# Performance work log

Hardware: AMD Instinct MI355X
Metric: run time of the kernel (lower is better)

The kernel has to match this reference:

```python
import jax, jax.numpy as jnp
import numpy as np
import math

BIG, SMALL, HEADS, FF_MULT = 4096, 256, 4, 2
HEAD_DIM = SMALL // HEADS
FF = SMALL * FF_MULT
EPS = 1.1920929e-07  # torch.nn.RMSNorm default eps=None -> finfo(float32).eps


def rmsnorm(x, g):
    var = jnp.mean(x * x, axis=-1, keepdims=True)
    return x * jax.lax.rsqrt(var + EPS) * g


def setup_inputs() -> dict:
    key = jax.random.key(0)
    ks = jax.random.split(key, 10)
    B, T = 4, 2048
    def lin(k, out_d, in_d):
        # torch nn.Linear default init: U(-1/sqrt(in), 1/sqrt(in)), weight shape (out, in)
        lim = 1.0 / math.sqrt(in_d)
        return jax.random.uniform(k, (out_d, in_d), jnp.float32, -lim, lim)
    return {
        "x": jax.random.normal(ks[0], (B, T, BIG), jnp.float32),
        "W_down": lin(ks[1], SMALL, BIG),
        "W_up": lin(ks[2], BIG, SMALL),
        "W_qkv": lin(ks[3], 3 * SMALL, SMALL),
        "W_o": lin(ks[4], SMALL, SMALL),
        "W_gate": lin(ks[5], FF, SMALL),
        "W_upff": lin(ks[6], FF, SMALL),
        "W_downff": lin(ks[7], SMALL, FF),
        "g1": jnp.ones((SMALL,), jnp.float32),
        "g2": jnp.ones((SMALL,), jnp.float32),
    }


def reference(x, W_down, W_up, W_qkv, W_o, W_gate, W_upff, W_downff, g1, g2):
    B, T, _ = x.shape
    h = x @ W_down.T                                     # (B,T,small)
    hn = rmsnorm(h, g1)
    qkv = (hn @ W_qkv.T).reshape(B, T, 3, HEADS, HEAD_DIM)
    qkv = jnp.transpose(qkv, (2, 0, 3, 1, 4))            # (3,B,H,T,hd)
    q, k, v = qkv[0], qkv[1], qkv[2]
    scores = jnp.einsum('bhqd,bhkd->bhqk', q, k) / math.sqrt(HEAD_DIM)
    causal = jnp.tril(jnp.ones((T, T), bool))
    scores = jnp.where(causal, scores, -jnp.inf)
    attn = jax.nn.softmax(scores, axis=-1)
    out = jnp.einsum('bhqk,bhkd->bhqd', attn, v)
    out = jnp.transpose(out, (0, 2, 1, 3)).reshape(B, T, SMALL)
    h = h + out @ W_o.T
    hn = rmsnorm(h, g2)
    ff = (jax.nn.silu(hn @ W_gate.T) * (hn @ W_upff.T)) @ W_downff.T
    h = h + ff
    return h @ W_up.T                                    # (B,T,big)
```

## Files before the change

### kernel.cpp

```cpp
#include <hip/hip_runtime.h>
#include <hip/hip_bf16.h>

typedef __bf16 bf16x8 __attribute__((ext_vector_type(8)));
typedef __bf16 bf16x4 __attribute__((ext_vector_type(4)));
typedef float f32x4 __attribute__((ext_vector_type(4)));

#define MFMA_BF16(a, b, c) __builtin_amdgcn_mfma_f32_16x16x32_bf16((a), (b), (c), 0, 0, 0)

__device__ __forceinline__ void g2lds16(void* lds, const void* g) {
  __builtin_amdgcn_global_load_lds(
      (const __attribute__((address_space(1))) void*)g,
      (__attribute__((address_space(3))) void*)lds, 16, 0, 0);
}

enum { EP_BF16 = 0, EP_F32 = 1, EP_ADD_F32 = 2, EP_ADD_BF16OUT = 3 };

template <int EPI, bool AF32, bool SPLITK, int MT>
__global__ __launch_bounds__(256, 2) void gemm_nt_kernel(
    const void* __restrict__ Av, const __bf16* __restrict__ B, const int K,
    __bf16* __restrict__ Co, float* __restrict__ Cf, const int ldc)
{
  __shared__ __align__(16) __bf16 As[2][MT * 32];
  __shared__ __align__(16) __bf16 Bs[2][128 * 32];
  const int tid = threadIdx.x;
  const int wv = tid >> 6, lane = tid & 63;
  const int r16 = lane & 15, g4 = lane >> 4;
  const int row0 = blockIdx.y * MT, col0 = blockIdx.x * 128;
  const int wr = (MT == 128) ? (wv >> 1) * 64 : 0;
  const int wc = (MT == 128) ? (wv & 1) * 64 : wv * 32;
  const int NW = (MT == 128) ? 4 : 2;
  const int kz0 = SPLITK ? blockIdx.z * 512 : 0;

  f32x4 acc[4][(MT == 128) ? 4 : 2];
#pragma unroll
  for (int m = 0; m < 4; ++m)
#pragma unroll
    for (int n = 0; n < NW; ++n) acc[m][n] = f32x4{0.f, 0.f, 0.f, 0.f};

  auto stage = [&](int buf, int k0) {
    if constexpr (AF32) {
      const float* A = (const float*)Av;
#pragma unroll
      for (int rr = 0; rr < 2; ++rr) {
        const int u = rr * 256 + tid;
        const int row = u >> 2, cg = ((u & 3) ^ (row & 3)) * 8;
        const float* src = A + (size_t)(row0 + row) * K + k0 + cg;
        const f32x4 a0 = *(const f32x4*)src;
        const f32x4 a1 = *(const f32x4*)(src + 4);
        bf16x8 w;
#pragma unroll
        for (int j = 0; j < 4; ++j) { w[j] = (__bf16)a0[j]; w[4 + j] = (__bf16)a1[j]; }
        *(bf16x8*)&As[buf][u * 8] = w;
      }
    } else {
      const __bf16* A = (const __bf16*)Av;
#pragma unroll
      for (int rr = 0; rr < (MT == 128 ? 2 : 1); ++rr) {
        const int u = rr * 256 + tid;
        const int row = u >> 2, cg = ((u & 3) ^ (row & 3)) * 8;
        g2lds16(&As[buf][u * 8], A + (size_t)(row0 + row) * K + k0 + cg);
      }
    }
#pragma unroll
    for (int rr = 0; rr < 2; ++rr) {
      const int u = rr * 256 + tid;
      const int row = u >> 2, cg = ((u & 3) ^ (row & 3)) * 8;
      g2lds16(&Bs[buf][u * 8], B + (size_t)(col0 + row) * K + k0 + cg);
    }
  };

  const int nk = SPLITK ? 16 : (K >> 5);
  int cur = 0;
  stage(0, kz0);
  __syncthreads();

  const int csw = (g4 ^ (r16 & 3)) * 8;
  for (int t = 0; t < nk; ++t) {
    if (t + 1 < nk) stage(cur ^ 1, kz0 + (t + 1) * 32);
    bf16x8 af[4], bfr[(MT == 128) ? 4 : 2];
#pragma unroll
    for (int m = 0; m < 4; ++m)
      af[m] = *(const bf16x8*)&As[cur][(wr + m * 16 + r16) * 32 + csw];
#pragma unroll
    for (int n = 0; n < NW; ++n)
      bfr[n] = *(const bf16x8*)&Bs[cur][(wc + n * 16 + r16) * 32 + csw];
#pragma unroll
    for (int m = 0; m < 4; ++m)
#pragma unroll
      for (int n = 0; n < NW; ++n)
        acc[m][n] = MFMA_BF16(af[m], bfr[n], acc[m][n]);
    __syncthreads();
    cur ^= 1;
  }

  const size_t zoff = SPLITK ? (size_t)blockIdx.z * 2097152 : 0;
#pragma unroll
  for (int m = 0; m < 4; ++m)
#pragma unroll
    for (int n = 0; n < NW; ++n)
#pragma unroll
      for (int r = 0; r < 4; ++r) {
        const int row = row0 + wr + m * 16 + g4 * 4 + r;
        const int col = col0 + wc + n * 16 + r16;
        const size_t idx = (size_t)row * ldc + col;
        const float v = acc[m][n][r];
        if constexpr (EPI == EP_BF16) Co[idx] = (__bf16)v;
        else if constexpr (EPI == EP_F32) Cf[zoff + idx] = v;
        else if constexpr (EPI == EP_ADD_F32) Cf[idx] += v;
        else Co[idx] = (__bf16)(Cf[idx] + v);
      }
}

__global__ void reduce8_kernel(const float* __restrict__ part, float* __restrict__ h)
{
  const size_t i = ((size_t)blockIdx.x * 256 + threadIdx.x) * 4;
  f32x4 s = *(const f32x4*)(part + i);
#pragma unroll
  for (int z = 1; z < 8; ++z) {
    const f32x4 p = *(const f32x4*)(part + (size_t)z * 2097152 + i);
#pragma unroll
    for (int j = 0; j < 4; ++j) s[j] += p[j];
  }
  *(f32x4*)(h + i) = s;
}

__global__ void cvt_kernel(const float* __restrict__ src, __bf16* __restrict__ dst, int n)
{
  const int i = (blockIdx.x * blockDim.x + threadIdx.x) * 4;
  if (i < n) {
    const f32x4 v = *(const f32x4*)(src + i);
    bf16x4 o;
#pragma unroll
    for (int j = 0; j < 4; ++j) o[j] = (__bf16)v[j];
    *(bf16x4*)(dst + i) = o;
  }
}

__global__ void rmsnorm_kernel(const float* __restrict__ h, const float* __restrict__ g,
                               __bf16* __restrict__ out)
{
  const int wv = threadIdx.x >> 6, lane = threadIdx.x & 63;
  const size_t row = (size_t)blockIdx.x * 4 + wv;
  const f32x4 v = *(const f32x4*)(h + row * 256 + lane * 4);
  float s = v[0] * v[0] + v[1] * v[1] + v[2] * v[2] + v[3] * v[3];
#pragma unroll
  for (int off = 1; off < 64; off <<= 1) s += __shfl_xor(s, off);
  const float scale = rsqrtf(s * (1.f / 256.f) + 1.1920929e-07f);
  const f32x4 gv = *(const f32x4*)(g + lane * 4);
  bf16x4 o;
#pragma unroll
  for (int j = 0; j < 4; ++j) o[j] = (__bf16)(v[j] * scale * gv[j]);
  *(bf16x4*)(out + row * 256 + lane * 4) = o;
}

__global__ void silumul_kernel(const __bf16* __restrict__ gate, const __bf16* __restrict__ up,
                               __bf16* __restrict__ out)
{
  const size_t i = ((size_t)blockIdx.x * blockDim.x + threadIdx.x) * 8;
  const bf16x8 gv = *(const bf16x8*)(gate + i);
  const bf16x8 uv = *(const bf16x8*)(up + i);
  bf16x8 ov;
#pragma unroll
  for (int j = 0; j < 8; ++j) {
    const float x = (float)gv[j];
    ov[j] = (__bf16)((x / (1.f + __expf(-x))) * (float)uv[j]);
  }
  *(bf16x8*)(out + i) = ov;
}

__global__ __launch_bounds__(256, 4) void attn_kernel(
    const __bf16* __restrict__ qkv, float* __restrict__ opart, float* __restrict__ lpart)
{
  const int bh = blockIdx.x;
  const int by = blockIdx.y;
  const int qb = (by < 16) ? (31 - by) : (by - 16);
  const int z = blockIdx.z;
  const int b = bh >> 2, hh = bh & 3;
  const int tid = threadIdx.x, wv = tid >> 6, lane = tid & 63;
  const int r16 = lane & 15, g4 = lane >> 4;
  const __bf16* base = qkv + (size_t)b * 2048 * 768;
  const int q0 = qb * 64;

  __shared__ __align__(16) __bf16 Ks[2][64 * 64];
  __shared__ __align__(16) __bf16 Vt[64 * 72];
  __shared__ __align__(16) __bf16 Ps[4][16 * 72];

  bf16x8 qf[2];
  {
    const __bf16* qrow = base + (size_t)(q0 + wv * 16 + r16) * 768 + hh * 64;
    qf[0] = *(const bf16x8*)(qrow + g4 * 8);
    qf[1] = *(const bf16x8*)(qrow + 32 + g4 * 8);
  }

  f32x4 oacc[4];
#pragma unroll
  for (int t = 0; t < 4; ++t) oacc[t] = f32x4{0.f, 0.f, 0.f, 0.f};
  float lsum[4] = {0.f, 0.f, 0.f, 0.f};

  auto stageK = [&](int buf, int kv0) {
#pragma unroll
    for (int rr = 0; rr < 2; ++rr) {
      const int u = rr * 256 + tid;
      const int kv = u >> 3, c = u & 7;
      g2lds16(&Ks[buf][u * 8],
              base + (size_t)(kv0 + kv) * 768 + 256 + hh * 64 + ((c ^ (kv & 7)) * 8));
    }
  };
  const int vrow = tid >> 2, vdg = (tid & 3) * 16;
  const int va_ = vrow >> 3, vb_ = vrow & 7;

  bf16x8 v0r, v1r;
  auto loadV = [&](int kv0) {
    const __bf16* vsrc = base + (size_t)(kv0 + vrow) * 768 + 512 + hh * 64 + vdg;
    v0r = *(const bf16x8*)vsrc;
    v1r = *(const bf16x8*)(vsrc + 8);
  };
  auto writeVt = [&]() {
#pragma unroll
    for (int i = 0; i < 8; ++i) {
      int d = vdg + i;
      Vt[d * 72 + ((va_ ^ (d >> 3)) << 3) + vb_] = v0r[i];
      d = vdg + 8 + i;
      Vt[d * 72 + ((va_ ^ (d >> 3)) << 3) + vb_] = v1r[i];
    }
  };

  int c = z, cur = 0;
  const bool any = (c <= qb);
  if (any) { stageK(0, c * 64); loadV(c * 64); }
  __syncthreads();
  if (any) writeVt();
  __syncthreads();

  while (c <= qb) {
    const int nxt = c + 2;
    if (nxt <= qb) { stageK(cur ^ 1, nxt * 64); loadV(nxt * 64); }

    f32x4 sacc[4];
#pragma unroll
    for (int t = 0; t < 4; ++t) sacc[t] = f32x4{0.f, 0.f, 0.f, 0.f};
#pragma unroll
    for (int t = 0; t < 4; ++t)
#pragma unroll
      for (int kk = 0; kk < 2; ++kk) {
        const bf16x8 kf = *(const bf16x8*)
            &Ks[cur][(t * 16 + r16) * 64 + (((kk * 4 + g4) ^ (r16 & 7)) * 8)];
        sacc[t] = MFMA_BF16(qf[kk], kf, sacc[t]);
      }

    const bool diag = (c == qb);
#pragma unroll
    for (int t = 0; t < 4; ++t)
#pragma unroll
      for (int r = 0; r < 4; ++r) {
        float p = __expf(sacc[t][r] * 0.125f);
        if (diag && (t * 16 + r16 > wv * 16 + g4 * 4 + r)) p = 0.f;
        lsum[r] += p;
        Ps[wv][(g4 * 4 + r) * 72 + t * 16 + r16] = (__bf16)p;
      }
    bf16x8 pa[2];
    pa[0] = *(const bf16x8*)&Ps[wv][r16 * 72 + g4 * 8];
    pa[1] = *(const bf16x8*)&Ps[wv][r16 * 72 + 32 + g4 * 8];

#pragma unroll
    for (int t2 = 0; t2 < 4; ++t2)
#pragma unroll
      for (int kk = 0; kk < 2; ++kk) {
        const int d = t2 * 16 + r16;
        const bf16x8 vf = *(const bf16x8*)
            &Vt[d * 72 + (((kk * 4 + g4) ^ (d >> 3)) * 8)];
        oacc[t2] = MFMA_BF16(pa[kk], vf, oacc[t2]);
      }

    __syncthreads();
    if (nxt <= qb) writeVt();
    __syncthreads();
    c = nxt;
    cur ^= 1;
  }

#pragma unroll
  for (int r = 0; r < 4; ++r) {
    lsum[r] += __shfl_xor(lsum[r], 1);
    lsum[r] += __shfl_xor(lsum[r], 2);
    lsum[r] += __shfl_xor(lsum[r], 4);
    lsum[r] += __shfl_xor(lsum[r], 8);
  }
  const size_t pb = (size_t)(bh * 32 + qb) * 2 + z;
  float* op = opart + pb * 4096;
#pragma unroll
  for (int t2 = 0; t2 < 4; ++t2)
#pragma unroll
    for (int r = 0; r < 4; ++r)
      op[(wv * 16 + g4 * 4 + r) * 64 + t2 * 16 + r16] = oacc[t2][r];
  if (r16 == 0) {
    float* lp = lpart + pb * 64;
#pragma unroll
    for (int r = 0; r < 4; ++r) lp[wv * 16 + g4 * 4 + r] = lsum[r];
  }
}

__global__ void attn_merge_kernel(const float* __restrict__ opart,
                                  const float* __restrict__ lpart,
                                  __bf16* __restrict__ ao)
{
  const int gid = blockIdx.x * 256 + threadIdx.x;
  const int col4 = (gid & 63) * 4;
  const int row_t = gid >> 6;
  const int b = row_t >> 11, row = row_t & 2047;
  const int qb = row >> 6, rloc = row & 63;
  const int hh = col4 >> 6, d = col4 & 63;
  const size_t p0 = ((size_t)((b * 4 + hh) * 32 + qb)) * 2;
  const f32x4 o0 = *(const f32x4*)(opart + p0 * 4096 + rloc * 64 + d);
  const f32x4 o1 = *(const f32x4*)(opart + (p0 + 1) * 4096 + rloc * 64 + d);
  const float inv = 1.f / (lpart[p0 * 64 + rloc] + lpart[(p0 + 1) * 64 + rloc]);
  bf16x4 o;
#pragma unroll
  for (int j = 0; j < 4; ++j) o[j] = (__bf16)((o0[j] + o1[j]) * inv);
  *(bf16x4*)(ao + (size_t)row_t * 256 + col4) = o;
}

extern "C" void kernel_launch(void* const* d_in, const int* in_sizes, int n_in,
                              void* d_out, int out_size, void* d_ws, size_t ws_size,
                              hipStream_t stream) {
  (void)in_sizes; (void)n_in; (void)out_size; (void)ws_size;
  const float* x     = (const float*)d_in[0];
  const float* Wdown = (const float*)d_in[1];
  const float* Wup   = (const float*)d_in[2];
  const float* Wqkv  = (const float*)d_in[3];
  const float* Wo    = (const float*)d_in[4];
  const float* Wgate = (const float*)d_in[5];
  const float* Wupff = (const float*)d_in[6];
  const float* Wdff  = (const float*)d_in[7];
  const float* g1    = (const float*)d_in[8];
  const float* g2    = (const float*)d_in[9];
  float* out = (float*)d_out;

  const size_t MB = 1 << 20;
  char* ws = (char*)d_ws;
  float*  h  = (float*)ws;
  __bf16* hn = (__bf16*)(ws + 8 * MB);
  __bf16* ao = (__bf16*)(ws + 12 * MB);
  __bf16* wb_down = (__bf16*)(ws + 16 * MB);
  __bf16* wb_up   = (__bf16*)(ws + 18 * MB);
  __bf16* wb_qkv  = (__bf16*)(ws + 20 * MB);
  __bf16* wb_o    = (__bf16*)(ws + 20 * MB + 384 * 1024);
  __bf16* wb_gate = (__bf16*)(ws + 20 * MB + 512 * 1024);
  __bf16* wb_upff = (__bf16*)(ws + 20 * MB + 768 * 1024);
  __bf16* wb_dff  = (__bf16*)(ws + 21 * MB);
  __bf16* hb = ao;

  char* ob = (char*)d_out;
  __bf16* qkv  = (__bf16*)(ob);
  __bf16* gate = (__bf16*)(ob + 12 * MB);
  __bf16* up   = (__bf16*)(ob + 20 * MB);
  float* hpart = (float*)(ob + 28 * MB);
  float* opart = (float*)(ob + 92 * MB);
  float* lpart = (float*)(ob + 112 * MB);
  __bf16* ffmid = gate;

  cvt_kernel<<<1024, 256, 0, stream>>>(Wdown, wb_down, 1048576);
  cvt_kernel<<<1024, 256, 0, stream>>>(Wup,   wb_up,   1048576);
  cvt_kernel<<<192, 256, 0, stream>>>(Wqkv,  wb_qkv,  196608);
  cvt_kernel<<<64,  256, 0, stream>>>(Wo,    wb_o,    65536);
  cvt_kernel<<<128, 256, 0, stream>>>(Wgate, wb_gate, 131072);
  cvt_kernel<<<128, 256, 0, stream>>>(Wupff, wb_upff, 131072);
  cvt_kernel<<<128, 256, 0, stream>>>(Wdff,  wb_dff,  131072);

  gemm_nt_kernel<EP_F32, true, true, 128><<<dim3(2, 64, 8), 256, 0, stream>>>(
      x, wb_down, 4096, nullptr, hpart, 256);
  reduce8_kernel<<<2048, 256, 0, stream>>>(hpart, h);

  rmsnorm_kernel<<<2048, 256, 0, stream>>>(h, g1, hn);
  gemm_nt_kernel<EP_BF16, false, false, 64><<<dim3(6, 128), 256, 0, stream>>>(
      hn, wb_qkv, 256, qkv, nullptr, 768);
  attn_kernel<<<dim3(16, 32, 2), 256, 0, stream>>>(qkv, opart, lpart);
  attn_merge_kernel<<<2048, 256, 0, stream>>>(opart, lpart, ao);
  gemm_nt_kernel<EP_ADD_F32, false, false, 64><<<dim3(2, 128), 256, 0, stream>>>(
      ao, wb_o, 256, nullptr, h, 256);
  rmsnorm_kernel<<<2048, 256, 0, stream>>>(h, g2, hn);
  gemm_nt_kernel<EP_BF16, false, false, 64><<<dim3(4, 128), 256, 0, stream>>>(
      hn, wb_gate, 256, gate, nullptr, 512);
  gemm_nt_kernel<EP_BF16, false, false, 64><<<dim3(4, 128), 256, 0, stream>>>(
      hn, wb_upff, 256, up, nullptr, 512);
  silumul_kernel<<<2048, 256, 0, stream>>>(gate, up, ffmid);
  gemm_nt_kernel<EP_ADD_BF16OUT, false, false, 64><<<dim3(2, 128), 256, 0, stream>>>(
      ffmid, wb_dff, 512, hb, h, 256);
  gemm_nt_kernel<EP_F32, false, false, 128><<<dim3(32, 64), 256, 0, stream>>>(
      hb, wb_up, 256, nullptr, out, 4096);
}
```

Before: 227.4 us.

## Fuse kernel launches and register-prefetch A tiles in GEMM pipeline

Merges the seven weight-cast launches into one kernel and fuses the split-K reduction with the first RMSNorm. The gate and up projections run as a single GEMM (relying on wb_gate and wb_upff being contiguous), and SiLU-multiply moves into the A-load of the down-FF GEMM. For fp32 and SiLU A sources, a two-deep register prefetch replaces the synchronous convert-then-store staging. The aim is fewer launches and less intermediate traffic, at the cost of more registers in the GEMM kernel and a dependence on the weight-buffer layout.

```diff
diff --git a/kernel.cpp b/kernel.cpp
--- a/kernel.cpp
+++ b/kernel.cpp
@@ -14,8 +14,9 @@
 }
 
 enum { EP_BF16 = 0, EP_F32 = 1, EP_ADD_F32 = 2, EP_ADD_BF16OUT = 3 };
-
-template <int EPI, bool AF32, bool SPLITK, int MT>
+enum { AS_BF16 = 0, AS_F32 = 1, AS_SILU = 2 };
+
+template <int EPI, int ASRC, bool SPLITK, int MT>
 __global__ __launch_bounds__(256, 2) void gemm_nt_kernel(
     const void* __restrict__ Av, const __bf16* __restrict__ B, const int K,
     __bf16* __restrict__ Co, float* __restrict__ Cf, const int ldc)
@@ -28,56 +29,83 @@
   const int row0 = blockIdx.y * MT, col0 = blockIdx.x * 128;
   const int wr = (MT == 128) ? (wv >> 1) * 64 : 0;
   const int wc = (MT == 128) ? (wv & 1) * 64 : wv * 32;
-  const int NW = (MT == 128) ? 4 : 2;
+  constexpr int NW = (MT == 128) ? 4 : 2;
+  constexpr int NA = (MT == 128) ? 2 : 1;
   const int kz0 = SPLITK ? blockIdx.z * 512 : 0;
 
-  f32x4 acc[4][(MT == 128) ? 4 : 2];
+  f32x4 acc[4][NW];
 #pragma unroll
   for (int m = 0; m < 4; ++m)
 #pragma unroll
     for (int n = 0; n < NW; ++n) acc[m][n] = f32x4{0.f, 0.f, 0.f, 0.f};
 
-  auto stage = [&](int buf, int k0) {
-    if constexpr (AF32) {
+  f32x4 pA[2][NA], pB[2][NA];
+  bf16x8 pg[2][NA], pu[2][NA];
+
+  auto loadA = [&](int slot, int k0) {
+    if constexpr (ASRC == AS_F32) {
       const float* A = (const float*)Av;
 #pragma unroll
-      for (int rr = 0; rr < 2; ++rr) {
-        const int u = rr * 256 + tid;
-        const int row = u >> 2, cg = ((u & 3) ^ (row & 3)) * 8;
+      for (int rr = 0; rr < NA; ++rr) {
+        const int u = rr * 256 + tid, row = u >> 2, cg = ((u & 3) ^ (row & 3)) * 8;
         const float* src = A + (size_t)(row0 + row) * K + k0 + cg;
-        const f32x4 a0 = *(const f32x4*)src;
-        const f32x4 a1 = *(const f32x4*)(src + 4);
-        bf16x8 w;
-#pragma unroll
-        for (int j = 0; j < 4; ++j) { w[j] = (__bf16)a0[j]; w[4 + j] = (__bf16)a1[j]; }
-        *(bf16x8*)&As[buf][u * 8] = w;
-      }
-    } else {
-      const __bf16* A = (const __bf16*)Av;
-#pragma unroll
-      for (int rr = 0; rr < (MT == 128 ? 2 : 1); ++rr) {
-        const int u = rr * 256 + tid;
-        const int row = u >> 2, cg = ((u & 3) ^ (row & 3)) * 8;
-        g2lds16(&As[buf][u * 8], A + (size_t)(row0 + row) * K + k0 + cg);
-      }
-    }
+        pA[slot][rr] = *(const f32x4*)src;
+        pB[slot][rr] = *(const f32x4*)(src + 4);
+      }
+    } else if constexpr (ASRC == AS_SILU) {
+      const __bf16* G = (const __bf16*)Av;
+#pragma unroll
+      for (int rr = 0; rr < NA; ++rr) {
+        const int u = rr * 256 + tid, row = u >> 2, cg = ((u & 3) ^ (row & 3)) * 8;
+        const __bf16* src = G + (size_t)(row0 + row) * 1024 + k0 + cg;
+        pg[slot][rr] = *(const bf16x8*)src;
+        pu[slot][rr] = *(const bf16x8*)(src + 512);
+      }
+    }
+  };
+  auto writeA = [&](int slot, int buf) {
+#pragma unroll
+    for (int rr = 0; rr < NA; ++rr) {
+      const int u = rr * 256 + tid;
+      bf16x8 w;
+      if constexpr (ASRC == AS_F32) {
+#pragma unroll
+        for (int j = 0; j < 4; ++j) {
+          w[j] = (__bf16)pA[slot][rr][j];
+          w[4 + j] = (__bf16)pB[slot][rr][j];
+        }
+      } else {
+#pragma unroll
+        for (int j = 0; j < 8; ++j) {
+          const float g = (float)pg[slot][rr][j];
+          w[j] = (__bf16)((g / (1.f + __expf(-g))) * (float)pu[slot][rr][j]);
+        }
+      }
+      *(bf16x8*)&As[buf][u * 8] = w;
+    }
+  };
+  auto stageA_lds = [&](int buf, int k0) {
+    const __bf16* A = (const __bf16*)Av;
+#pragma unroll
+    for (int rr = 0; rr < NA; ++rr) {
+      const int u = rr * 256 + tid, row = u >> 2, cg = ((u & 3) ^ (row & 3)) * 8;
+      g2lds16(&As[buf][u * 8], A + (size_t)(row0 + row) * K + k0 + cg);
+    }
+  };
+  auto stageB = [&](int buf, int k0) {
 #pragma unroll
     for (int rr = 0; rr < 2; ++rr) {
-      const int u = rr * 256 + tid;
-      const int row = u >> 2, cg = ((u & 3) ^ (row & 3)) * 8;
+      const int u = rr * 256 + tid, row = u >> 2, cg = ((u & 3) ^ (row & 3)) * 8;
       g2lds16(&Bs[buf][u * 8], B + (size_t)(col0 + row) * K + k0 + cg);
     }
   };
 
   const int nk = SPLITK ? 16 : (K >> 5);
+  const int csw = (g4 ^ (r16 & 3)) * 8;
   int cur = 0;
-  stage(0, kz0);
-  __syncthreads();
-
-  const int csw = (g4 ^ (r16 & 3)) * 8;
-  for (int t = 0; t < nk; ++t) {
-    if (t + 1 < nk) stage(cur ^ 1, kz0 + (t + 1) * 32);
-    bf16x8 af[4], bfr[(MT == 128) ? 4 : 2];
+
+  auto compute = [&]() {
+    bf16x8 af[4], bfr[NW];
 #pragma unroll
     for (int m = 0; m < 4; ++m)
       af[m] = *(const bf16x8*)&As[cur][(wr + m * 16 + r16) * 32 + csw];
@@ -89,8 +117,32 @@
 #pragma unroll
       for (int n = 0; n < NW; ++n)
         acc[m][n] = MFMA_BF16(af[m], bfr[n], acc[m][n]);
+  };
+
+  if constexpr (ASRC == AS_BF16) {
+    stageA_lds(0, kz0);
+    stageB(0, kz0);
     __syncthreads();
-    cur ^= 1;
+    for (int t = 0; t < nk; ++t) {
+      if (t + 1 < nk) { stageA_lds(cur ^ 1, kz0 + (t + 1) * 32); stageB(cur ^ 1, kz0 + (t + 1) * 32); }
+      compute();
+      __syncthreads();
+      cur ^= 1;
+    }
+  } else {
+    loadA(0, kz0);
+    if (nk > 1) loadA(1, kz0 + 32);
+    stageB(0, kz0);
+    writeA(0, 0);
+    __syncthreads();
+    for (int t = 0; t < nk; ++t) {
+      if (t + 2 < nk) loadA(t & 1, kz0 + (t + 2) * 32);
+      if (t + 1 < nk) stageB(cur ^ 1, kz0 + (t + 1) * 32);
+      compute();
+      if (t + 1 < nk) writeA((t + 1) & 1, cur ^ 1);
+      __syncthreads();
+      cur ^= 1;
+    }
   }
 
   const size_t zoff = SPLITK ? (size_t)blockIdx.z * 2097152 : 0;
@@ -111,29 +163,29 @@
       }
 }
 
-__global__ void reduce8_kernel(const float* __restrict__ part, float* __restrict__ h)
-{
-  const size_t i = ((size_t)blockIdx.x * 256 + threadIdx.x) * 4;
-  f32x4 s = *(const f32x4*)(part + i);
+__global__ void rmsnorm_reduce_kernel(const float* __restrict__ part, const float* __restrict__ g,
+                                      float* __restrict__ h, __bf16* __restrict__ out)
+{
+  const int wv = threadIdx.x >> 6, lane = threadIdx.x & 63;
+  const size_t row = (size_t)blockIdx.x * 4 + wv;
+  const size_t i = row * 256 + lane * 4;
+  f32x4 v = *(const f32x4*)(part + i);
 #pragma unroll
   for (int z = 1; z < 8; ++z) {
     const f32x4 p = *(const f32x4*)(part + (size_t)z * 2097152 + i);
 #pragma unroll
-    for (int j = 0; j < 4; ++j) s[j] += p[j];
-  }
-  *(f32x4*)(h + i) = s;
-}
-
-__global__ void cvt_kernel(const float* __restrict__ src, __bf16* __restrict__ dst, int n)
-{
-  const int i = (blockIdx.x * blockDim.x + threadIdx.x) * 4;
-  if (i < n) {
-    const f32x4 v = *(const f32x4*)(src + i);
-    bf16x4 o;
-#pragma unroll
-    for (int j = 0; j < 4; ++j) o[j] = (__bf16)v[j];
-    *(bf16x4*)(dst + i) = o;
-  }
+    for (int j = 0; j < 4; ++j) v[j] += p[j];
+  }
+  *(f32x4*)(h + i) = v;
+  float s = v[0] * v[0] + v[1] * v[1] + v[2] * v[2] + v[3] * v[3];
+#pragma unroll
+  for (int off = 1; off < 64; off <<= 1) s += __shfl_xor(s, off);
+  const float scale = rsqrtf(s * (1.f / 256.f) + 1.1920929e-07f);
+  const f32x4 gv = *(const f32x4*)(g + lane * 4);
+  bf16x4 o;
+#pragma unroll
+  for (int j = 0; j < 4; ++j) o[j] = (__bf16)(v[j] * scale * gv[j]);
+  *(bf16x4*)(out + i) = o;
 }
 
 __global__ void rmsnorm_kernel(const float* __restrict__ h, const float* __restrict__ g,
@@ -153,19 +205,22 @@
   *(bf16x4*)(out + row * 256 + lane * 4) = o;
 }
 
-__global__ void silumul_kernel(const __bf16* __restrict__ gate, const __bf16* __restrict__ up,
-                               __bf16* __restrict__ out)
-{
-  const size_t i = ((size_t)blockIdx.x * blockDim.x + threadIdx.x) * 8;
-  const bf16x8 gv = *(const bf16x8*)(gate + i);
-  const bf16x8 uv = *(const bf16x8*)(up + i);
-  bf16x8 ov;
-#pragma unroll
-  for (int j = 0; j < 8; ++j) {
-    const float x = (float)gv[j];
-    ov[j] = (__bf16)((x / (1.f + __expf(-x))) * (float)uv[j]);
-  }
-  *(bf16x8*)(out + i) = ov;
+struct CvtPack { const float* s[7]; __bf16* d[7]; int n[7]; };
+__global__ void cvt_all_kernel(CvtPack p)
+{
+  int i = (blockIdx.x * 256 + threadIdx.x) * 4;
+#pragma unroll
+  for (int k = 0; k < 7; ++k) {
+    if (i < p.n[k]) {
+      const f32x4 v = *(const f32x4*)(p.s[k] + i);
+      bf16x4 o;
+#pragma unroll
+      for (int j = 0; j < 4; ++j) o[j] = (__bf16)v[j];
+      *(bf16x4*)(p.d[k] + i) = o;
+      return;
+    }
+    i -= p.n[k];
+  }
 }
 
 __global__ __launch_bounds__(256, 4) void attn_kernel(
@@ -352,40 +407,36 @@
 
   char* ob = (char*)d_out;
   __bf16* qkv  = (__bf16*)(ob);
-  __bf16* gate = (__bf16*)(ob + 12 * MB);
-  __bf16* up   = (__bf16*)(ob + 20 * MB);
+  __bf16* gu   = (__bf16*)(ob + 12 * MB);
   float* hpart = (float*)(ob + 28 * MB);
   float* opart = (float*)(ob + 92 * MB);
   float* lpart = (float*)(ob + 112 * MB);
-  __bf16* ffmid = gate;
-
-  cvt_kernel<<<1024, 256, 0, stream>>>(Wdown, wb_down, 1048576);
-  cvt_kernel<<<1024, 256, 0, stream>>>(Wup,   wb_up,   1048576);
-  cvt_kernel<<<192, 256, 0, stream>>>(Wqkv,  wb_qkv,  196608);
-  cvt_kernel<<<64,  256, 0, stream>>>(Wo,    wb_o,    65536);
-  cvt_kernel<<<128, 256, 0, stream>>>(Wgate, wb_gate, 131072);
-  cvt_kernel<<<128, 256, 0, stream>>>(Wupff, wb_upff, 131072);
-  cvt_kernel<<<128, 256, 0, stream>>>(Wdff,  wb_dff,  131072);
-
-  gemm_nt_kernel<EP_F32, true, true, 128><<<dim3(2, 64, 8), 256, 0, stream>>>(
+
+  CvtPack cp;
+  cp.s[0] = Wdown; cp.d[0] = wb_down; cp.n[0] = 1048576;
+  cp.s[1] = Wup;   cp.d[1] = wb_up;   cp.n[1] = 1048576;
+  cp.s[2] = Wqkv;  cp.d[2] = wb_qkv;  cp.n[2] = 196608;
+  cp.s[3] = Wo;    cp.d[3] = wb_o;    cp.n[3] = 65536;
+  cp.s[4] = Wgate; cp.d[4] = wb_gate; cp.n[4] = 131072;
+  cp.s[5] = Wupff; cp.d[5] = wb_upff; cp.n[5] = 131072;
+  cp.s[6] = Wdff;  cp.d[6] = wb_dff;  cp.n[6] = 131072;
+  cvt_all_kernel<<<2688, 256, 0, stream>>>(cp);
+
+  gemm_nt_kernel<EP_F32, AS_F32, true, 128><<<dim3(2, 64, 8), 256, 0, stream>>>(
       x, wb_down, 4096, nullptr, hpart, 256);
-  reduce8_kernel<<<2048, 256, 0, stream>>>(hpart, h);
-
-  rmsnorm_kernel<<<2048, 256, 0, stream>>>(h, g1, hn);
-  gemm_nt_kernel<EP_BF16, false, false, 64><<<dim3(6, 128), 256, 0, stream>>>(
+  rmsnorm_reduce_kernel<<<2048, 256, 0, stream>>>(hpart, g1, h, hn);
+
+  gemm_nt_kernel<EP_BF16, AS_BF16, false, 64><<<dim3(6, 128), 256, 0, stream>>>(
       hn, wb_qkv, 256, qkv, nullptr, 768);
   attn_kernel<<<dim3(16, 32, 2), 256, 0, stream>>>(qkv, opart, lpart);
   attn_merge_kernel<<<2048, 256, 0, stream>>>(opart, lpart, ao);
-  gemm_nt_kernel<EP_ADD_F32, false, false, 64><<<dim3(2, 128), 256, 0, stream>>>(
+  gemm_nt_kernel<EP_ADD_F32, AS_BF16, false, 64><<<dim3(2, 128), 256, 0, stream>>>(
       ao, wb_o, 256, nullptr, h, 256);
   rmsnorm_kernel<<<2048, 256, 0, stream>>>(h, g2, hn);
-  gemm_nt_kernel<EP_BF16, false, false, 64><<<dim3(4, 128), 256, 0, stream>>>(
-      hn, wb_gate, 256, gate, nullptr, 512);
-  gemm_nt_kernel<EP_BF16, false, false, 64><<<dim3(4, 128), 256, 0, stream>>>(
-      hn, wb_upff, 256, up, nullptr, 512);
-  silumul_kernel<<<2048, 256, 0, stream>>>(gate, up, ffmid);
-  gemm_nt_kernel<EP_ADD_BF16OUT, false, false, 64><<<dim3(2, 128), 256, 0, stream>>>(
-      ffmid, wb_dff, 512, hb, h, 256);
-  gemm_nt_kernel<EP_F32, false, false, 128><<<dim3(32, 64), 256, 0, stream>>>(
+  gemm_nt_kernel<EP_BF16, AS_BF16, false, 64><<<dim3(8, 128), 256, 0, stream>>>(
+      hn, wb_gate, 256, gu, nullptr, 1024);
+  gemm_nt_kernel<EP_ADD_BF16OUT, AS_SILU, false, 64><<<dim3(2, 128), 256, 0, stream>>>(
+      gu, wb_dff, 512, hb, h, 256);
+  gemm_nt_kernel<EP_F32, AS_BF16, false, 128><<<dim3(32, 64), 256, 0, stream>>>(
       hb, wb_up, 256, nullptr, out, 4096);
 }
```

Result: slower. 246.7 us (+8.5%).
